# Performance work log

Measured on AMD Instinct MI355X. Metric: run time of the kernel, lower is better.

Reference implementation:

```python
import jax, jax.numpy as jnp
import numpy as np

DIM = 768
HEADS = 12
HEAD_DIM = DIM // HEADS
SCALE = HEAD_DIM ** -0.5


def setup_inputs() -> dict:
    key = jax.random.key(0)
    k1, k2, k3, k4, k5 = jax.random.split(key, 5)
    B, N = 4, 2048
    x = jax.random.normal(k1, (B, N, DIM), dtype=jnp.float32)
    # qkv Linear: weight [3*dim, dim], bias [3*dim]
    w_qkv = jax.random.normal(k2, (3 * DIM, DIM), dtype=jnp.float32) * (DIM ** -0.5)
    b_qkv = jax.random.normal(k3, (3 * DIM,), dtype=jnp.float32) * 0.01
    # proj Linear: weight [dim, dim], bias [dim]
    w_proj = jax.random.normal(k4, (DIM, DIM), dtype=jnp.float32) * (DIM ** -0.5)
    b_proj = jax.random.normal(k5, (DIM,), dtype=jnp.float32) * 0.01
    return {"x": x, "w_qkv": w_qkv, "b_qkv": b_qkv, "w_proj": w_proj, "b_proj": b_proj}


def reference(x, w_qkv, b_qkv, w_proj, b_proj):
    B, N, C = x.shape
    qkv = (jnp.einsum('bnc,oc->bno', x, w_qkv) + b_qkv)
    qkv = qkv.reshape(B, N, 3, HEADS, HEAD_DIM).transpose(2, 0, 3, 1, 4)
    q, k, v = qkv[0], qkv[1], qkv[2]
    attn = jnp.einsum('bhqd,bhkd->bhqk', q, k) * SCALE
    attn = jax.nn.softmax(attn, axis=-1)
    out = jnp.einsum('bhqk,bhkd->bhqd', attn, v)  # [B, H, N, Dh]
    out = out.transpose(0, 2, 1, 3).reshape(B, N, C)
    # dropout is identity in eval mode
    return jnp.einsum('bnc,oc->bno', out, w_proj) + b_proj
```

## Files before the change

kernel.cpp:

```cpp
#include <hip/hip_runtime.h>
#include <hip/hip_bf16.h>

using bf16 = __hip_bfloat16;
typedef __bf16 bf16x8 __attribute__((ext_vector_type(8)));
typedef short short4v __attribute__((ext_vector_type(4)));
typedef short short8v __attribute__((ext_vector_type(8)));
typedef float float4v __attribute__((ext_vector_type(4)));

#define DIM   768
#define NH    12
#define HD    64
#define SEQ   2048
#define BATCH 4
#define TOK   (BATCH * SEQ)
#define SCALE_QL2E 0.18033688011112042f

#define NX  (TOK * DIM)
#define NWQ (3 * DIM * DIM)
#define NWP (DIM * DIM)

__device__ __forceinline__ short f2bf(float f) {
  union { bf16 h; short s; } u;
  u.h = __float2bfloat16(f);
  return u.s;
}

union frag8 { short4v h[2]; short8v s; bf16x8 b; };

__device__ __forceinline__ void async_copy16(const bf16* g, short* l) {
  __builtin_amdgcn_global_load_lds(
      (const __attribute__((address_space(1))) unsigned int*)g,
      (__attribute__((address_space(3))) unsigned int*)l, 16, 0, 0);
}
__device__ __forceinline__ void async_copy4(const bf16* g, short* l) {
  __builtin_amdgcn_global_load_lds(
      (const __attribute__((address_space(1))) unsigned int*)g,
      (__attribute__((address_space(3))) unsigned int*)l, 4, 0, 0);
}

__global__ void __launch_bounds__(256)
cvt3(const float* __restrict__ a, bf16* __restrict__ oa, long na,
     const float* __restrict__ b, bf16* __restrict__ ob, long nb,
     const float* __restrict__ c, bf16* __restrict__ oc, long nc) {
  const long i = ((long)blockIdx.x * 256 + threadIdx.x) * 8;
  const float* src; bf16* dst; long off;
  if (i < na)                { src = a; dst = oa; off = i; }
  else if (i < na + nb)      { src = b; dst = ob; off = i - na; }
  else if (i < na + nb + nc) { src = c; dst = oc; off = i - na - nb; }
  else return;
  const float4v x0 = *(const float4v*)(src + off);
  const float4v x1 = *(const float4v*)(src + off + 4);
  short8v r;
  r[0] = f2bf(x0[0]); r[1] = f2bf(x0[1]); r[2] = f2bf(x0[2]); r[3] = f2bf(x0[3]);
  r[4] = f2bf(x1[0]); r[5] = f2bf(x1[1]); r[6] = f2bf(x1[2]); r[7] = f2bf(x1[3]);
  *(short8v*)(dst + off) = r;
}

__device__ __forceinline__ void gemm_mainloop(const bf16* __restrict__ A,
                                              const bf16* __restrict__ B,
                                              short* As, short* Bs,
                                              float4v acc[4][4]) {
  const int t = threadIdx.x;
  const int w = t >> 6, l = t & 63, lr = l & 15, q = l >> 4;
  const int wr = ((w >> 1) << 6), wc = ((w & 1) << 6);

  const bf16* Ag = A + (t >> 2) * DIM + (t & 3) * 8;
  const bf16* Bg = B + (t >> 2) * DIM + (t & 3) * 8;

  for (int k0 = 0; k0 < DIM; k0 += 32) {
    __syncthreads();
    async_copy16(Ag,            &As[t * 8]);
    async_copy16(Ag + 64 * DIM, &As[2048 + t * 8]);
    async_copy16(Bg,            &Bs[t * 8]);
    async_copy16(Bg + 64 * DIM, &Bs[2048 + t * 8]);
    Ag += 32; Bg += 32;
    __syncthreads();

    bf16x8 af[4], bfv[4];
#pragma unroll
    for (int i = 0; i < 4; ++i)
      af[i] = *(const bf16x8*)&As[(wr + i * 16 + lr) * 32 + q * 8];
#pragma unroll
    for (int j = 0; j < 4; ++j)
      bfv[j] = *(const bf16x8*)&Bs[(wc + j * 16 + lr) * 32 + q * 8];
#pragma unroll
    for (int i = 0; i < 4; ++i)
#pragma unroll
      for (int j = 0; j < 4; ++j)
        acc[i][j] = __builtin_amdgcn_mfma_f32_16x16x32_bf16(af[i], bfv[j],
                                                            acc[i][j], 0, 0, 0);
  }
}

#define VW5 asm volatile("s_waitcnt vmcnt(5)" ::: "memory")
#define VW0 asm volatile("s_waitcnt vmcnt(0)" ::: "memory")
#define BARRIER __builtin_amdgcn_s_barrier()
#define LGKM0 asm volatile("s_waitcnt lgkmcnt(0)" ::: "memory")
#define NOSTG (void)0
#define NOVW  (void)0

#define STGP(s, p)                                                            \
  async_copy16(pa + (p) * 32,             &As[s][t * 8]);                     \
  async_copy16(pa + 128 * DIM + (p) * 32, &As[s][4096 + t * 8]);              \
  async_copy16(pb + (p) * 32,             &Bs[s][t * 8]);                     \
  async_copy16(pb + 128 * DIM + (p) * 32, &Bs[s][4096 + t * 8]);              \
  async_copy4 (pb3 + (p) * 32,            &Bs[s][8192 + t * 2])

#define PHASE(RS, STG_, VW_) {                                                \
  bf16x8 af[4], bfv[9];                                                       \
  _Pragma("unroll") for (int mf_ = 0; mf_ < 4; ++mf_)                         \
    af[mf_] = *(const bf16x8*)&As[RS][mf_ * 512 + arow];                      \
  _Pragma("unroll") for (int nf_ = 0; nf_ < 9; ++nf_)                         \
    bfv[nf_] = *(const bf16x8*)&Bs[RS][nf_ * 512 + brow];                     \
  STG_; BARRIER; LGKM0;                                                       \
  __builtin_amdgcn_s_setprio(1);                                              \
  _Pragma("unroll") for (int mf_ = 0; mf_ < 4; ++mf_)                         \
  _Pragma("unroll") for (int nf_ = 0; nf_ < 9; ++nf_)                         \
    acc[mf_][nf_] = __builtin_amdgcn_mfma_f32_16x16x32_bf16(                  \
        af[mf_], bfv[nf_], acc[mf_][nf_], 0, 0, 0);                           \
  __builtin_amdgcn_s_setprio(0); VW_; BARRIER; }

__global__ void __launch_bounds__(512, 2)
gemm_qkv(const bf16* __restrict__ X, const bf16* __restrict__ W,
         const float* __restrict__ bias,
         bf16* __restrict__ qb, bf16* __restrict__ kb, bf16* __restrict__ vb) {
  __shared__ short As[3][256 * 32];
  __shared__ short Bs[3][288 * 32];
  const int t = threadIdx.x;
  const int w = t >> 6, l = t & 63, lr = l & 15, q = l >> 4;
  const int wm = w >> 1, wn = w & 1;

  const int orig = blockIdx.x;
  const int swz = (orig & 7) * 32 + (orig >> 3);
  const int tm = swz >> 3, tn = swz & 7;
  const int row0 = tm * 256, col0 = tn * 288;

  const int sr = t >> 2;
  const int scol = (((t & 3) << 3) ^ (((sr >> 1) & 3) << 3));
  const bf16* pa  = X + (size_t)(row0 + sr) * DIM + scol;
  const bf16* pb  = W + (size_t)(col0 + sr) * DIM + scol;
  const int r3 = 256 + (t >> 4);
  const int c3 = ((t & 15) << 1) ^ (((r3 >> 1) & 3) << 3);
  const bf16* pb3 = W + (size_t)(col0 + r3) * DIM + c3;

  const int acol = ((q << 3) ^ (((lr >> 1) & 3) << 3));
  const int arow = (wm * 64 + lr) * 32 + acol;
  const int brow = (wn * 144 + lr) * 32 + acol;

  float4v acc[4][9] = {};

  STGP(0, 0);
  STGP(1, 1);
  VW5; BARRIER;

  PHASE(0, STGP(2, 2),  VW5)
  PHASE(1, STGP(0, 3),  VW5)
  PHASE(2, STGP(1, 4),  VW5)
  PHASE(0, STGP(2, 5),  VW5)
  PHASE(1, STGP(0, 6),  VW5)
  PHASE(2, STGP(1, 7),  VW5)
  PHASE(0, STGP(2, 8),  VW5)
  PHASE(1, STGP(0, 9),  VW5)
  PHASE(2, STGP(1, 10), VW5)
  PHASE(0, STGP(2, 11), VW5)
  PHASE(1, STGP(0, 12), VW5)
  PHASE(2, STGP(1, 13), VW5)
  PHASE(0, STGP(2, 14), VW5)
  PHASE(1, STGP(0, 15), VW5)
  PHASE(2, STGP(1, 16), VW5)
  PHASE(0, STGP(2, 17), VW5)
  PHASE(1, STGP(0, 18), VW5)
  PHASE(2, STGP(1, 19), VW5)
  PHASE(0, STGP(2, 20), VW5)
  PHASE(1, STGP(0, 21), VW5)
  PHASE(2, STGP(1, 22), VW5)
  PHASE(0, STGP(2, 23), VW5)
  PHASE(1, NOSTG,       VW0)
  PHASE(2, NOSTG,       NOVW)

#pragma unroll
  for (int nf = 0; nf < 9; ++nf) {
    const int gn = col0 + wn * 144 + nf * 16 + lr;
    const int which = gn / DIM;
    const int cc = gn - which * DIM;
    const int hh = cc >> 6, dd = cc & 63;
    const float bv = bias[gn];
#pragma unroll
    for (int mf = 0; mf < 4; ++mf) {
      const int gm0 = row0 + wm * 64 + mf * 16 + (q << 2);
      const int b = gm0 >> 11, n0 = gm0 & 2047;
      if (which == 2) {
        short4v pv;
#pragma unroll
        for (int r = 0; r < 4; ++r) pv[r] = f2bf(acc[mf][nf][r] + bv);
        *(short4v*)&vb[((size_t)(b * NH + hh) * HD + dd) * SEQ + n0] = pv;
      } else {
        bf16* dst = (which == 0) ? qb : kb;
        const float sc = (which == 0) ? SCALE_QL2E : 1.0f;
#pragma unroll
        for (int r = 0; r < 4; ++r)
          dst[((size_t)(b * NH + hh) * SEQ + n0 + r) * HD + dd] =
              __float2bfloat16((acc[mf][nf][r] + bv) * sc);
      }
    }
  }
}

__global__ void __launch_bounds__(256, 3)
flash_attn(const bf16* __restrict__ Qp, const bf16* __restrict__ Kp,
           const bf16* __restrict__ Vtp, bf16* __restrict__ Op) {
  const int bh = blockIdx.y, qt = blockIdx.x;
  const int t = threadIdx.x, w = t >> 6, l = t & 63, lr = l & 15, q = l >> 4;
  __shared__ short Ks[2][64 * 68];
  __shared__ short Vt[2][64 * 66];

  const bf16* Qb = Qp  + (size_t)(bh * SEQ + qt * 128) * HD;
  const bf16* Kb = Kp  + (size_t)bh * SEQ * HD;
  const bf16* Vb = Vtp + (size_t)bh * HD * SEQ;

  const int tr3 = t >> 3, td8 = (t & 7) * 8;

#pragma unroll
  for (int i = 0; i < 4; ++i) {
    const int row = i * 32 + tr3;
    *(short8v*)&Ks[row >> 6][(row & 63) * 68 + td8] =
        *(const short8v*)(Qb + (size_t)row * HD + td8);
  }
  __syncthreads();
  bf16x8 qf[2][2];
#pragma unroll
  for (int it = 0; it < 2; ++it)
#pragma unroll
    for (int kq = 0; kq < 2; ++kq) {
      const int row = w * 32 + it * 16 + lr;
      qf[it][kq] = *(const bf16x8*)&Ks[row >> 6][(row & 63) * 68 + kq * 32 + q * 8];
    }
  __syncthreads();

  short8v kr[2], vr[2];
#pragma unroll
  for (int i = 0; i < 2; ++i) {
    kr[i] = *(const short8v*)(Kb + (size_t)(i * 32 + tr3) * HD + td8);
    vr[i] = *(const short8v*)(Vb + (size_t)(i * 32 + tr3) * SEQ + td8);
  }

  frag8 ones;
#pragma unroll
  for (int r = 0; r < 8; ++r) ones.s[r] = (short)0x3F80;

  float4v o[2][4] = {};
  float4v lacc[2] = {};

  for (int kt = 0; kt < 32; ++kt) {
    const int cur = kt & 1;
#pragma unroll
    for (int i = 0; i < 2; ++i) {
      *(short8v*)&Ks[cur][(i * 32 + tr3) * 68 + td8] = kr[i];
      *(short8v*)&Vt[cur][(i * 32 + tr3) * 66 + td8] = vr[i];
    }
    if (kt < 31) {
      const int k1 = (kt + 1) * 64;
#pragma unroll
      for (int i = 0; i < 2; ++i) {
        kr[i] = *(const short8v*)(Kb + (size_t)(k1 + i * 32 + tr3) * HD + td8);
        vr[i] = *(const short8v*)(Vb + (size_t)(i * 32 + tr3) * SEQ + k1 + td8);
      }
    }
    __syncthreads();

    float4v s[4][2] = {};
    __builtin_amdgcn_s_setprio(1);
#pragma unroll
    for (int jn = 0; jn < 4; ++jn) {
      bf16x8 kf[2];
#pragma unroll
      for (int kq = 0; kq < 2; ++kq)
        kf[kq] = *(const bf16x8*)&Ks[cur][(jn * 16 + lr) * 68 + kq * 32 + q * 8];
#pragma unroll
      for (int it = 0; it < 2; ++it)
#pragma unroll
        for (int kq = 0; kq < 2; ++kq)
          s[jn][it] = __builtin_amdgcn_mfma_f32_16x16x32_bf16(kf[kq], qf[it][kq],
                                                              s[jn][it], 0, 0, 0);
    }
    __builtin_amdgcn_s_setprio(0);

    frag8 pf[2][2];
#pragma unroll
    for (int it = 0; it < 2; ++it)
#pragma unroll
      for (int c4 = 0; c4 < 2; ++c4)
#pragma unroll
        for (int r = 0; r < 4; ++r) {
          pf[c4][it].s[r]     = f2bf(__builtin_amdgcn_exp2f(s[2 * c4][it][r]));
          pf[c4][it].s[4 + r] = f2bf(__builtin_amdgcn_exp2f(s[2 * c4 + 1][it][r]));
        }

    __builtin_amdgcn_s_setprio(1);
#pragma unroll
    for (int c4 = 0; c4 < 2; ++c4) {
#pragma unroll
      for (int dj = 0; dj < 4; ++dj) {
        frag8 vf;
        vf.h[0] = *(const short4v*)&Vt[cur][(dj * 16 + lr) * 66 + c4 * 32 + (q << 2)];
        vf.h[1] = *(const short4v*)&Vt[cur][(dj * 16 + lr) * 66 + c4 * 32 + 16 + (q << 2)];
#pragma unroll
        for (int it = 0; it < 2; ++it)
          o[it][dj] = __builtin_amdgcn_mfma_f32_16x16x32_bf16(pf[c4][it].b, vf.b,
                                                              o[it][dj], 0, 0, 0);
      }
#pragma unroll
      for (int it = 0; it < 2; ++it)
        lacc[it] = __builtin_amdgcn_mfma_f32_16x16x32_bf16(pf[c4][it].b, ones.b,
                                                           lacc[it], 0, 0, 0);
    }
    __builtin_amdgcn_s_setprio(0);
  }

  const int b = bh / NH, h = bh - b * NH;
#pragma unroll
  for (int it = 0; it < 2; ++it)
#pragma unroll
    for (int r = 0; r < 4; ++r) {
      const float linv = 1.0f / lacc[it][r];
      const int grow = b * SEQ + qt * 128 + w * 32 + it * 16 + (q << 2) + r;
      bf16* orow = Op + (size_t)grow * DIM + h * HD;
#pragma unroll
      for (int dj = 0; dj < 4; ++dj)
        orow[dj * 16 + lr] = __float2bfloat16(o[it][dj][r] * linv);
    }
}

__global__ void __launch_bounds__(256)
gemm_proj(const bf16* __restrict__ A, const bf16* __restrict__ W,
          const float* __restrict__ bias, float* __restrict__ out) {
  __shared__ short As[128 * 32];
  __shared__ short Bs[128 * 32];
  const int t = threadIdx.x;
  const int w = t >> 6, l = t & 63, lr = l & 15, q = l >> 4;
  const int wr = ((w >> 1) << 6), wc = ((w & 1) << 6);
  const int row0 = blockIdx.y * 128, col0 = blockIdx.x * 128;

  float4v acc[4][4] = {};
  gemm_mainloop(A + row0 * DIM, W + col0 * DIM, As, Bs, acc);

#pragma unroll
  for (int j = 0; j < 4; ++j) {
    const int gn = col0 + wc + j * 16 + lr;
    const float bv = bias[gn];
#pragma unroll
    for (int i = 0; i < 4; ++i) {
#pragma unroll
      for (int r = 0; r < 4; ++r) {
        const int gm = row0 + wr + i * 16 + (q << 2) + r;
        out[(size_t)gm * DIM + gn] = acc[i][j][r] + bv;
      }
    }
  }
}

extern "C" void kernel_launch(void* const* d_in, const int* in_sizes, int n_in,
                              void* d_out, int out_size, void* d_ws, size_t ws_size,
                              hipStream_t stream) {
  const float* x      = (const float*)d_in[0];
  const float* w_qkv  = (const float*)d_in[1];
  const float* b_qkv  = (const float*)d_in[2];
  const float* w_proj = (const float*)d_in[3];
  const float* b_proj = (const float*)d_in[4];
  float* out = (float*)d_out;

  const size_t perbuf = (size_t)BATCH * NH * SEQ * HD;
  bf16* qb  = (bf16*)d_ws;
  bf16* kb  = qb + perbuf;
  bf16* vb  = kb + perbuf;
  bf16* ao  = vb + perbuf;
  bf16* xb  = ao + perbuf;
  bf16* wqb = xb + (size_t)NX;
  bf16* wpb = wqb + (size_t)NWQ;

  const int cvt_blocks = (NX + NWQ + NWP) / 8 / 256;
  cvt3<<<cvt_blocks, 256, 0, stream>>>(x, xb, NX, w_qkv, wqb, NWQ, w_proj, wpb, NWP);
  gemm_qkv <<<dim3(256), 512, 0, stream>>>(xb, wqb, b_qkv, qb, kb, vb);
  flash_attn<<<dim3(SEQ / 128, BATCH * NH), 256, 0, stream>>>(qb, kb, vb, ao);
  gemm_proj <<<dim3(DIM / 128, TOK / 128),  256, 0, stream>>>(ao, wpb, b_proj, out);
}
```

Baseline: 207.8 us.

## Shrink QKV GEMM tile to 128x288 with 256 threads and double buffering

The QKV projection GEMM moves from 256x288 tiles with 512 threads and triple-buffered LDS to 128x288 tiles with 256 threads and double buffering. The grid doubles to 512 blocks, and the K loop becomes a rolled loop that waits for all loads each phase (vmcnt 0). The aim is to cut LDS use and raise block count for better occupancy and wave balance. In exchange it gives up the deeper prefetch and the overlap of loads with MFMA work, and it reloads the weight tile per smaller row tile.

After: 205.8 us. About the same (-1.0%).

```diff
diff --git a/kernel.cpp b/kernel.cpp
--- a/kernel.cpp
+++ b/kernel.cpp
@@ -92,7 +92,6 @@
   }
 }
 
-#define VW5 asm volatile("s_waitcnt vmcnt(5)" ::: "memory")
 #define VW0 asm volatile("s_waitcnt vmcnt(0)" ::: "memory")
 #define BARRIER __builtin_amdgcn_s_barrier()
 #define LGKM0 asm volatile("s_waitcnt lgkmcnt(0)" ::: "memory")
@@ -101,17 +100,20 @@
 
 #define STGP(s, p)                                                            \
   async_copy16(pa + (p) * 32,             &As[s][t * 8]);                     \
-  async_copy16(pa + 128 * DIM + (p) * 32, &As[s][4096 + t * 8]);              \
+  async_copy16(pa + 64 * DIM + (p) * 32,  &As[s][2048 + t * 8]);              \
   async_copy16(pb + (p) * 32,             &Bs[s][t * 8]);                     \
+  async_copy16(pb + 64 * DIM + (p) * 32,  &Bs[s][2048 + t * 8]);              \
   async_copy16(pb + 128 * DIM + (p) * 32, &Bs[s][4096 + t * 8]);              \
-  async_copy4 (pb3 + (p) * 32,            &Bs[s][8192 + t * 2])
-
-#define PHASE(RS, STG_, VW_) {                                                \
+  async_copy16(pb + 192 * DIM + (p) * 32, &Bs[s][6144 + t * 8]);              \
+  async_copy4 (pb3 + (p) * 32,            &Bs[s][8192 + t * 2]);              \
+  async_copy4 (pb3 + 16 * DIM + (p) * 32, &Bs[s][8704 + t * 2])
+
+#define PHASE(CUR, STG_, VW_) {                                               \
   bf16x8 af[4], bfv[9];                                                       \
   _Pragma("unroll") for (int mf_ = 0; mf_ < 4; ++mf_)                         \
-    af[mf_] = *(const bf16x8*)&As[RS][mf_ * 512 + arow];                      \
+    af[mf_] = *(const bf16x8*)&As[CUR][mf_ * 512 + arow];                     \
   _Pragma("unroll") for (int nf_ = 0; nf_ < 9; ++nf_)                         \
-    bfv[nf_] = *(const bf16x8*)&Bs[RS][nf_ * 512 + brow];                     \
+    bfv[nf_] = *(const bf16x8*)&Bs[CUR][nf_ * 512 + brow];                    \
   STG_; BARRIER; LGKM0;                                                       \
   __builtin_amdgcn_s_setprio(1);                                              \
   _Pragma("unroll") for (int mf_ = 0; mf_ < 4; ++mf_)                         \
@@ -120,28 +122,28 @@
         af[mf_], bfv[nf_], acc[mf_][nf_], 0, 0, 0);                           \
   __builtin_amdgcn_s_setprio(0); VW_; BARRIER; }
 
-__global__ void __launch_bounds__(512, 2)
+__global__ void __launch_bounds__(256, 2)
 gemm_qkv(const bf16* __restrict__ X, const bf16* __restrict__ W,
          const float* __restrict__ bias,
          bf16* __restrict__ qb, bf16* __restrict__ kb, bf16* __restrict__ vb) {
-  __shared__ short As[3][256 * 32];
-  __shared__ short Bs[3][288 * 32];
+  __shared__ short As[2][128 * 32];
+  __shared__ short Bs[2][288 * 32];
   const int t = threadIdx.x;
   const int w = t >> 6, l = t & 63, lr = l & 15, q = l >> 4;
   const int wm = w >> 1, wn = w & 1;
 
   const int orig = blockIdx.x;
-  const int swz = (orig & 7) * 32 + (orig >> 3);
+  const int swz = (orig & 7) * 64 + (orig >> 3);
   const int tm = swz >> 3, tn = swz & 7;
-  const int row0 = tm * 256, col0 = tn * 288;
+  const int row0 = tm * 128, col0 = tn * 288;
 
   const int sr = t >> 2;
   const int scol = (((t & 3) << 3) ^ (((sr >> 1) & 3) << 3));
   const bf16* pa  = X + (size_t)(row0 + sr) * DIM + scol;
   const bf16* pb  = W + (size_t)(col0 + sr) * DIM + scol;
-  const int r3 = 256 + (t >> 4);
+  const int r3 = t >> 4;
   const int c3 = ((t & 15) << 1) ^ (((r3 >> 1) & 3) << 3);
-  const bf16* pb3 = W + (size_t)(col0 + r3) * DIM + c3;
+  const bf16* pb3 = W + (size_t)(col0 + 256 + r3) * DIM + c3;
 
   const int acol = ((q << 3) ^ (((lr >> 1) & 3) << 3));
   const int arow = (wm * 64 + lr) * 32 + acol;
@@ -150,33 +152,15 @@
   float4v acc[4][9] = {};
 
   STGP(0, 0);
-  STGP(1, 1);
-  VW5; BARRIER;
-
-  PHASE(0, STGP(2, 2),  VW5)
-  PHASE(1, STGP(0, 3),  VW5)
-  PHASE(2, STGP(1, 4),  VW5)
-  PHASE(0, STGP(2, 5),  VW5)
-  PHASE(1, STGP(0, 6),  VW5)
-  PHASE(2, STGP(1, 7),  VW5)
-  PHASE(0, STGP(2, 8),  VW5)
-  PHASE(1, STGP(0, 9),  VW5)
-  PHASE(2, STGP(1, 10), VW5)
-  PHASE(0, STGP(2, 11), VW5)
-  PHASE(1, STGP(0, 12), VW5)
-  PHASE(2, STGP(1, 13), VW5)
-  PHASE(0, STGP(2, 14), VW5)
-  PHASE(1, STGP(0, 15), VW5)
-  PHASE(2, STGP(1, 16), VW5)
-  PHASE(0, STGP(2, 17), VW5)
-  PHASE(1, STGP(0, 18), VW5)
-  PHASE(2, STGP(1, 19), VW5)
-  PHASE(0, STGP(2, 20), VW5)
-  PHASE(1, STGP(0, 21), VW5)
-  PHASE(2, STGP(1, 22), VW5)
-  PHASE(0, STGP(2, 23), VW5)
-  PHASE(1, NOSTG,       VW0)
-  PHASE(2, NOSTG,       NOVW)
+  VW0; BARRIER;
+
+#pragma unroll 1
+  for (int k = 0; k < 22; k += 2) {
+    PHASE(0, STGP(1, k + 1), VW0)
+    PHASE(1, STGP(0, k + 2), VW0)
+  }
+  PHASE(0, STGP(1, 23), VW0)
+  PHASE(1, NOSTG,       NOVW)
 
 #pragma unroll
   for (int nf = 0; nf < 9; ++nf) {
@@ -380,7 +364,7 @@
 
   const int cvt_blocks = (NX + NWQ + NWP) / 8 / 256;
   cvt3<<<cvt_blocks, 256, 0, stream>>>(x, xb, NX, w_qkv, wqb, NWQ, w_proj, wpb, NWP);
-  gemm_qkv <<<dim3(256), 512, 0, stream>>>(xb, wqb, b_qkv, qb, kb, vb);
+  gemm_qkv <<<dim3(512), 256, 0, stream>>>(xb, wqb, b_qkv, qb, kb, vb);
   flash_attn<<<dim3(SEQ / 128, BATCH * NH), 256, 0, stream>>>(qb, kb, vb, ao);
   gemm_proj <<<dim3(DIM / 128, TOK / 128),  256, 0, stream>>>(ao, wpb, b_proj, out);
 }
```
